# Kernel optimization log

Hardware: AMD Instinct MI355X
Metric: run time of the kernel (lower is better)

Reference implementation:

```python
import jax, jax.numpy as jnp
import numpy as np

EMBED_DIM = 1024
NUM_HEADS = 16
HEAD_DIM = EMBED_DIM // NUM_HEADS


def setup_inputs() -> dict:
    key = jax.random.key(0)
    ks = jax.random.split(key, 7)
    B, S, D = 2, 2048, EMBED_DIM
    s = 1.0 / np.sqrt(D)
    return {
        "x": jax.random.normal(ks[0], (B, S, D), dtype=jnp.float32),
        "Wq": jax.random.normal(ks[1], (D, D), dtype=jnp.float32) * s,
        "bq": jax.random.normal(ks[2], (D,), dtype=jnp.float32) * 0.01,
        "Wk": jax.random.normal(ks[3], (D, D), dtype=jnp.float32) * s,
        "bk": jax.random.normal(ks[4], (D,), dtype=jnp.float32) * 0.01,
        "Wv": jax.random.normal(ks[5], (D, D), dtype=jnp.float32) * s,
        "bv": jax.random.normal(ks[6], (D,), dtype=jnp.float32) * 0.01,
    }


def reference(x, Wq, bq, Wk, bk, Wv, bv):
    B, S, D = x.shape
    H, Hd = NUM_HEADS, HEAD_DIM
    # QKV projections, then split heads: [B, S, D] -> [B, H, S, Hd]
    q = (x @ Wq + bq).reshape(B, S, H, Hd).transpose(0, 2, 1, 3)
    k = (x @ Wk + bk).reshape(B, S, H, Hd).transpose(0, 2, 1, 3)
    v = (x @ Wv + bv).reshape(B, S, H, Hd).transpose(0, 2, 1, 3)
    # NOTE: the original module applies NO 1/sqrt(head_dim) scaling.
    energy = jnp.einsum("bhqd,bhkd->bhqk", q, k)  # [B, H, S, S]
    attn = jax.nn.softmax(energy, axis=-1)
    out = jnp.einsum("bhqk,bhkd->bhqd", attn, v)
    return out.transpose(0, 2, 1, 3).reshape(B, S, D)
```

## Files before the change

kernel.cpp:

```cpp
#include <hip/hip_runtime.h>
#include <stdint.h>
#include <stddef.h>

typedef _Float16 half_t;
typedef __attribute__((ext_vector_type(8))) _Float16 h16x8;
typedef __attribute__((ext_vector_type(4))) _Float16 h16x4;
typedef __attribute__((ext_vector_type(4))) float f32x4;

#define MFMA16(a, b, c) __builtin_amdgcn_mfma_f32_16x16x32_f16(a, b, c, 0, 0, 0)
#define EXP2(x) __builtin_amdgcn_exp2f(x)

#define SW(row, slot) ((((slot) ^ ((row) & 7))) * 8)

__device__ __forceinline__ void gload_lds16(const half_t* g, half_t* l) {
    __builtin_amdgcn_global_load_lds(
        (const __attribute__((address_space(1))) void*)g,
        (__attribute__((address_space(3))) void*)l, 16, 0, 0);
}

__global__ __launch_bounds__(256) void cvt_x_kernel(const float* __restrict__ x,
                                                    half_t* __restrict__ xh, int n8) {
    int i = blockIdx.x * blockDim.x + threadIdx.x;
    if (i >= n8) return;
    const float4* xv = (const float4*)x;
    float4 a = xv[i * 2 + 0];
    float4 b = xv[i * 2 + 1];
    h16x8 o;
    o[0] = (half_t)a.x; o[1] = (half_t)a.y; o[2] = (half_t)a.z; o[3] = (half_t)a.w;
    o[4] = (half_t)b.x; o[5] = (half_t)b.y; o[6] = (half_t)b.z; o[7] = (half_t)b.w;
    ((h16x8*)xh)[i] = o;
}

__global__ __launch_bounds__(256) void cvt_w_kernel(const float* __restrict__ Wq,
                                                    const float* __restrict__ Wk,
                                                    const float* __restrict__ Wv,
                                                    half_t* __restrict__ Wt) {
    __shared__ float t[32][33];
    const float* W = (blockIdx.z == 0) ? Wq : ((blockIdx.z == 1) ? Wk : Wv);
    int k0 = blockIdx.y * 32, n0 = blockIdx.x * 32;
    int tid = threadIdx.x;
    int r = tid >> 3;
    int c4 = (tid & 7) * 4;
    float4 v = *(const float4*)&W[(size_t)(k0 + r) * 1024 + n0 + c4];
    t[r][c4 + 0] = v.x; t[r][c4 + 1] = v.y; t[r][c4 + 2] = v.z; t[r][c4 + 3] = v.w;
    __syncthreads();
    half_t* o = Wt + (size_t)blockIdx.z * 1024 * 1024 + (size_t)(n0 + r) * 1024 + k0 + c4;
    h16x4 h;
    h[0] = (half_t)t[c4 + 0][r];
    h[1] = (half_t)t[c4 + 1][r];
    h[2] = (half_t)t[c4 + 2][r];
    h[3] = (half_t)t[c4 + 3][r];
    *(h16x4*)o = h;
}

__global__ __launch_bounds__(256, 3) void gemm_qkv_kernel(
    const half_t* __restrict__ xh,
    const half_t* __restrict__ Wt,
    const float* __restrict__ bq, const float* __restrict__ bk,
    const float* __restrict__ bv,
    half_t* __restrict__ qkv)
{
    const int p = blockIdx.z;
    const float* bias = (p == 0) ? bq : ((p == 1) ? bk : bv);
    const half_t* Wp = Wt + (size_t)p * 1024 * 1024;
    const int n0 = blockIdx.x * 128, m0 = blockIdx.y * 128;

    __shared__ half_t Al[128][64];
    __shared__ half_t Bl[128][64];

    const int tid = threadIdx.x;
    const int lane = tid & 63, wid = tid >> 6;
    const int wm = wid >> 1, wn = wid & 1;
    const int g = lane >> 4, r = lane & 15;

    const int lrow = lane >> 3;
    const int swzc = ((lane & 7) ^ lrow) * 8;

    f32x4 acc[4][4];
#pragma unroll
    for (int a = 0; a < 4; a++)
#pragma unroll
        for (int c = 0; c < 4; c++) acc[a][c] = (f32x4){0.f, 0.f, 0.f, 0.f};

    for (int k0 = 0; k0 < 1024; k0 += 64) {
        __syncthreads();
#pragma unroll
        for (int j = 0; j < 4; j++) {
            int issue = wid * 4 + j;
            int row = issue * 8 + lrow;
            gload_lds16(&xh[(size_t)(m0 + row) * 1024 + k0 + swzc], &Al[0][0] + issue * 512);
            gload_lds16(&Wp[(size_t)(n0 + row) * 1024 + k0 + swzc], &Bl[0][0] + issue * 512);
        }
        __syncthreads();

#pragma unroll
        for (int t = 0; t < 2; t++) {
            h16x8 af[4], bf[4];
#pragma unroll
            for (int mi = 0; mi < 4; mi++)
                af[mi] = *(const h16x8*)&Al[wm * 64 + mi * 16 + r][SW(r, t * 4 + g)];
#pragma unroll
            for (int ni = 0; ni < 4; ni++)
                bf[ni] = *(const h16x8*)&Bl[wn * 64 + ni * 16 + r][SW(r, t * 4 + g)];
#pragma unroll
            for (int mi = 0; mi < 4; mi++)
#pragma unroll
                for (int ni = 0; ni < 4; ni++)
                    acc[mi][ni] = MFMA16(af[mi], bf[ni], acc[mi][ni]);
        }
    }

    float bn[4];
#pragma unroll
    for (int ni = 0; ni < 4; ni++) bn[ni] = bias[n0 + wn * 64 + ni * 16 + r];

    if (p == 0) {
        half_t* outp = qkv;
#pragma unroll
        for (int mi = 0; mi < 4; mi++) {
#pragma unroll
            for (int ni = 0; ni < 4; ni++) {
                int n = n0 + wn * 64 + ni * 16 + r;
                int hq = n >> 6, hd = n & 63;
#pragma unroll
                for (int i = 0; i < 4; i++) {
                    int m = m0 + wm * 64 + mi * 16 + g * 4 + i;
                    int b = m >> 11, s = m & 2047;
                    outp[(((size_t)(b * 16 + hq) * 2048 + s) << 6) + hd] =
                        (half_t)(acc[mi][ni][i] + bn[ni]);
                }
            }
        }
    } else if (p == 1) {
        half_t* outp = qkv + (size_t)4194304;
        const int kt = ((m0 & 2047) + wm * 64) >> 6;
        const int bK = (m0 + wm * 64) >> 11;
#pragma unroll
        for (int ni = 0; ni < 4; ni++) {
            int n = n0 + wn * 64 + ni * 16 + r;
            int hK = n >> 6, hd = n & 63;
            int tt = hd >> 5, ggk = (hd >> 3) & 3, jK = hd & 7;
            size_t base = (size_t)(bK * 16 + hK) * 131072 + kt * 4096 + tt * 512 + ggk * 128 + jK;
#pragma unroll
            for (int mi = 0; mi < 4; mi++)
#pragma unroll
                for (int i = 0; i < 4; i++)
                    outp[base + mi * 1024 + (g * 4 + i) * 8] =
                        (half_t)(acc[mi][ni][i] + bn[ni]);
        }
    } else {
        half_t* outp = qkv + (size_t)2 * 4194304;
        const int kt = ((m0 & 2047) + wm * 64) >> 6;
        const int bV = (m0 + wm * 64) >> 11;
        const int jv = (g & 1) * 4, gv_hi = g >> 1;
#pragma unroll
        for (int ni = 0; ni < 4; ni++) {
            int n = n0 + wn * 64 + ni * 16 + r;
            int hV = n >> 6;
            size_t hb = (size_t)(bV * 16 + hV) * 131072 + kt * 4096 + ni * 1024;
#pragma unroll
            for (int mi = 0; mi < 4; mi++) {
                int ks = mi >> 1, ggv = (mi & 1) * 2 + gv_hi;
                h16x4 pk;
#pragma unroll
                for (int i = 0; i < 4; i++) pk[i] = (half_t)(acc[mi][ni][i] + bn[ni]);
                *(h16x4*)&outp[hb + ks * 512 + ggv * 128 + r * 8 + jv] = pk;
            }
        }
    }
}

__global__ __launch_bounds__(256, 2) void attn_kernel(
    const half_t* __restrict__ Qg,
    const half_t* __restrict__ Kswz,
    const half_t* __restrict__ Vswz,
    float* __restrict__ out)
{
    __shared__ half_t Pl[4][32][64];

    const int tid = threadIdx.x;
    const int lane = tid & 63, wid = tid >> 6;
    const int g = lane >> 4, r = lane & 15;

    const int bid = blockIdx.x;
    const int xcd = bid & 7;
    const int t_  = bid >> 3;
    const int qblk = t_ & 15;
    const int bh = xcd + 8 * (t_ >> 4);

    const int b = bh >> 4, h = bh & 15;
    const half_t* Qb = Qg + (size_t)bh * 131072;
    const half_t* Kp = Kswz + (size_t)bh * 131072;
    const half_t* Vp = Vswz + (size_t)bh * 131072;
    const int q0 = qblk * 128 + wid * 32;
    const int lofs = g * 128 + r * 8;

    h16x8 qf[2][2];
#pragma unroll
    for (int qg = 0; qg < 2; qg++)
#pragma unroll
        for (int t = 0; t < 2; t++) {
            qf[qg][t] = *(const h16x8*)&Qb[(size_t)(q0 + qg * 16 + r) * 64 + t * 32 + g * 8];
            qf[qg][t] *= (half_t)1.44269504f;
        }

    const h16x8 ones = {(half_t)1.f, (half_t)1.f, (half_t)1.f, (half_t)1.f,
                        (half_t)1.f, (half_t)1.f, (half_t)1.f, (half_t)1.f};

    f32x4 o[2][4], lsum[2];
#pragma unroll
    for (int qg = 0; qg < 2; qg++) {
#pragma unroll
        for (int d = 0; d < 4; d++) o[qg][d] = (f32x4){0.f, 0.f, 0.f, 0.f};
        lsum[qg] = (f32x4){0.f, 0.f, 0.f, 0.f};
    }
    float m_run[2] = {0.f, 0.f};

    h16x8 kf[8], vf[8];

    auto loadK = [&](int kt) {
#pragma unroll
        for (int kc = 0; kc < 4; kc++)
#pragma unroll
            for (int t = 0; t < 2; t++)
                kf[kc * 2 + t] = *(const h16x8*)&Kp[kt * 4096 + kc * 1024 + t * 512 + lofs];
    };
    auto loadV = [&](int kt) {
#pragma unroll
        for (int d = 0; d < 4; d++)
#pragma unroll
            for (int ks = 0; ks < 2; ks++)
                vf[d * 2 + ks] = *(const h16x8*)&Vp[kt * 4096 + d * 1024 + ks * 512 + lofs];
    };

    auto QKT = [&](f32x4 (&e)[2][4]) {
        __builtin_amdgcn_s_setprio(1);
#pragma unroll
        for (int kc = 0; kc < 4; kc++) {
            e[0][kc] = (f32x4){0.f, 0.f, 0.f, 0.f};
            e[1][kc] = (f32x4){0.f, 0.f, 0.f, 0.f};
#pragma unroll
            for (int t = 0; t < 2; t++) {
                e[0][kc] = MFMA16(kf[kc * 2 + t], qf[0][t], e[0][kc]);
                e[1][kc] = MFMA16(kf[kc * 2 + t], qf[1][t], e[1][kc]);
            }
        }
        __builtin_amdgcn_s_setprio(0);
    };

    auto SOFTMAX_P = [&](f32x4 (&e)[2][4]) {
#pragma unroll
        for (int qg = 0; qg < 2; qg++) {
            float t0 = fmaxf(fmaxf(e[qg][0][0], e[qg][0][1]), e[qg][0][2]);
            float t1 = fmaxf(fmaxf(e[qg][0][3], e[qg][1][0]), e[qg][1][1]);
            float t2 = fmaxf(fmaxf(e[qg][1][2], e[qg][1][3]), e[qg][2][0]);
            float t3 = fmaxf(fmaxf(e[qg][2][1], e[qg][2][2]), e[qg][2][3]);
            float t4 = fmaxf(fmaxf(e[qg][3][0], e[qg][3][1]), e[qg][3][2]);
            float tm = fmaxf(fmaxf(t0, t1), fmaxf(fmaxf(t2, t3), fmaxf(t4, e[qg][3][3])));
            tm = fmaxf(tm, __shfl_xor(tm, 16));
            tm = fmaxf(tm, __shfl_xor(tm, 32));

#pragma unroll
            for (int kc = 0; kc < 4; kc++)
#pragma unroll
                for (int i = 0; i < 4; i++) e[qg][kc][i] = EXP2(e[qg][kc][i] - m_run[qg]);

            if (!__all(tm <= m_run[qg] + 8.f)) {
                float nm = fmaxf(m_run[qg], tm);
                float sc = EXP2(m_run[qg] - nm);
                m_run[qg] = nm;
#pragma unroll
                for (int kc = 0; kc < 4; kc++)
#pragma unroll
                    for (int i = 0; i < 4; i++) e[qg][kc][i] *= sc;
#pragma unroll
                for (int i = 0; i < 4; i++) {
                    float sci = __shfl(sc, (lane & 48) | (g * 4 + i));
                    lsum[qg][i] *= sci;
#pragma unroll
                    for (int d = 0; d < 4; d++) o[qg][d][i] *= sci;
                }
            }

#pragma unroll
            for (int kc = 0; kc < 4; kc++) {
                h16x4 pk;
#pragma unroll
                for (int i = 0; i < 4; i++) pk[i] = (half_t)e[qg][kc][i];
                *(h16x4*)&Pl[wid][qg * 16 + r][SW(r, 2 * kc + (g >> 1)) + (g & 1) * 4] = pk;
            }
        }
    };

    auto PV = [&]() {
        asm volatile("s_waitcnt lgkmcnt(0)" ::: "memory");
        __builtin_amdgcn_sched_barrier(0);
        __builtin_amdgcn_s_setprio(1);
#pragma unroll
        for (int ks = 0; ks < 2; ks++) {
            h16x8 pf0 = *(const h16x8*)&Pl[wid][r][SW(r, ks * 4 + g)];
            h16x8 pf1 = *(const h16x8*)&Pl[wid][16 + r][SW(r, ks * 4 + g)];
#pragma unroll
            for (int d = 0; d < 4; d++) {
                o[0][d] = MFMA16(pf0, vf[d * 2 + ks], o[0][d]);
                o[1][d] = MFMA16(pf1, vf[d * 2 + ks], o[1][d]);
            }
            lsum[0] = MFMA16(pf0, ones, lsum[0]);
            lsum[1] = MFMA16(pf1, ones, lsum[1]);
        }
        __builtin_amdgcn_s_setprio(0);
    };

    f32x4 eA[2][4], eB[2][4];
    loadK(0);
    QKT(eA);
    loadK(1);

    for (int kt = 0; kt < 32; kt += 2) {
        loadV(kt);
        SOFTMAX_P(eA);
        QKT(eB);
        loadK((kt + 2) & 31);
        PV();
        loadV(kt + 1);
        SOFTMAX_P(eB);
        QKT(eA);
        loadK((kt + 3) & 31);
        PV();
    }

#pragma unroll
    for (int qg = 0; qg < 2; qg++)
#pragma unroll
        for (int i = 0; i < 4; i++) {
            float inv = 1.0f / lsum[qg][i];
            int s = q0 + qg * 16 + g * 4 + i;
            float* op = out + (size_t)(b * 2048 + s) * 1024 + h * 64 + r;
#pragma unroll
            for (int d = 0; d < 4; d++) op[d * 16] = o[qg][d][i] * inv;
        }
}

extern "C" void kernel_launch(void* const* d_in, const int* in_sizes, int n_in,
                              void* d_out, int out_size, void* d_ws, size_t ws_size,
                              hipStream_t stream) {
    const float* x  = (const float*)d_in[0];
    const float* Wq = (const float*)d_in[1];
    const float* bq = (const float*)d_in[2];
    const float* Wk = (const float*)d_in[3];
    const float* bk = (const float*)d_in[4];
    const float* Wv = (const float*)d_in[5];
    const float* bv = (const float*)d_in[6];
    float* out = (float*)d_out;

    half_t* xh  = (half_t*)d_ws;
    half_t* Wt  = (half_t*)((char*)d_ws + (size_t)8 * 1024 * 1024);
    half_t* qkv = (half_t*)((char*)d_ws + (size_t)14 * 1024 * 1024);
    half_t* Qh  = qkv;
    half_t* Kh  = qkv + (size_t)4194304;
    half_t* Vth = qkv + (size_t)8388608;

    cvt_x_kernel<<<2048, 256, 0, stream>>>(x, xh, 524288);
    cvt_w_kernel<<<dim3(32, 32, 3), 256, 0, stream>>>(Wq, Wk, Wv, Wt);
    gemm_qkv_kernel<<<dim3(8, 32, 3), 256, 0, stream>>>(xh, Wt, bq, bk, bv, qkv);
    attn_kernel<<<512, 256, 0, stream>>>(Qh, Kh, Vth, out);
}
```

Baseline: 98.65 us.

## Feed P to PV MFMA directly from registers, dropping LDS round-trip

Softmax probabilities are now kept in registers and fed straight to 16x16x16 MFMAs for the PV product, so the per-wave LDS staging buffer, its writes, waitcnt and reads are gone. The V output layout in the projection kernel is rearranged so the accumulator layout of QK^T matches the B operand of the K=16 MFMA. In exchange it doubles the number of PV MFMA instructions at half the K depth, and it reorders the pipeline so softmax runs after the next QK^T is issued.

```diff
diff --git a/kernel.cpp b/kernel.cpp
--- a/kernel.cpp
+++ b/kernel.cpp
@@ -7,7 +7,8 @@
 typedef __attribute__((ext_vector_type(4))) _Float16 h16x4;
 typedef __attribute__((ext_vector_type(4))) float f32x4;
 
-#define MFMA16(a, b, c) __builtin_amdgcn_mfma_f32_16x16x32_f16(a, b, c, 0, 0, 0)
+#define MFMA16(a, b, c)   __builtin_amdgcn_mfma_f32_16x16x32_f16(a, b, c, 0, 0, 0)
+#define MFMA16K16(a, b, c) __builtin_amdgcn_mfma_f32_16x16x16f16(a, b, c, 0, 0, 0)
 #define EXP2(x) __builtin_amdgcn_exp2f(x)
 
 #define SW(row, slot) ((((slot) ^ ((row) & 7))) * 8)
@@ -152,19 +153,16 @@
         half_t* outp = qkv + (size_t)2 * 4194304;
         const int kt = ((m0 & 2047) + wm * 64) >> 6;
         const int bV = (m0 + wm * 64) >> 11;
-        const int jv = (g & 1) * 4, gv_hi = g >> 1;
+        const int hV = (n0 + wn * 64) >> 6;
+        size_t base = (size_t)(bV * 16 + hV) * 131072 + kt * 4096 + (g * 16 + r) * 8;
 #pragma unroll
         for (int ni = 0; ni < 4; ni++) {
-            int n = n0 + wn * 64 + ni * 16 + r;
-            int hV = n >> 6;
-            size_t hb = (size_t)(bV * 16 + hV) * 131072 + kt * 4096 + ni * 1024;
 #pragma unroll
             for (int mi = 0; mi < 4; mi++) {
-                int ks = mi >> 1, ggv = (mi & 1) * 2 + gv_hi;
                 h16x4 pk;
 #pragma unroll
                 for (int i = 0; i < 4; i++) pk[i] = (half_t)(acc[mi][ni][i] + bn[ni]);
-                *(h16x4*)&outp[hb + ks * 512 + ggv * 128 + r * 8 + jv] = pk;
+                *(h16x4*)&outp[base + (ni * 2 + (mi >> 1)) * 512 + (mi & 1) * 4] = pk;
             }
         }
     }
@@ -176,10 +174,8 @@
     const half_t* __restrict__ Vswz,
     float* __restrict__ out)
 {
-    __shared__ half_t Pl[4][32][64];
-
     const int tid = threadIdx.x;
-    const int lane = tid & 63, wid = tid >> 6;
+    const int lane = tid & 63;
     const int g = lane >> 4, r = lane & 15;
 
     const int bid = blockIdx.x;
@@ -192,7 +188,7 @@
     const half_t* Qb = Qg + (size_t)bh * 131072;
     const half_t* Kp = Kswz + (size_t)bh * 131072;
     const half_t* Vp = Vswz + (size_t)bh * 131072;
-    const int q0 = qblk * 128 + wid * 32;
+    const int q0 = qblk * 128 + (tid >> 6) * 32;
     const int lofs = g * 128 + r * 8;
 
     h16x8 qf[2][2];
@@ -204,8 +200,7 @@
             qf[qg][t] *= (half_t)1.44269504f;
         }
 
-    const h16x8 ones = {(half_t)1.f, (half_t)1.f, (half_t)1.f, (half_t)1.f,
-                        (half_t)1.f, (half_t)1.f, (half_t)1.f, (half_t)1.f};
+    const h16x4 ones4 = {(half_t)1.f, (half_t)1.f, (half_t)1.f, (half_t)1.f};
 
     f32x4 o[2][4], lsum[2];
 #pragma unroll
@@ -227,10 +222,8 @@
     };
     auto loadV = [&](int kt) {
 #pragma unroll
-        for (int d = 0; d < 4; d++)
-#pragma unroll
-            for (int ks = 0; ks < 2; ks++)
-                vf[d * 2 + ks] = *(const h16x8*)&Vp[kt * 4096 + d * 1024 + ks * 512 + lofs];
+        for (int dh = 0; dh < 8; dh++)
+            vf[dh] = *(const h16x8*)&Vp[kt * 4096 + dh * 512 + lofs];
     };
 
     auto QKT = [&](f32x4 (&e)[2][4]) {
@@ -248,7 +241,8 @@
         __builtin_amdgcn_s_setprio(0);
     };
 
-    auto SOFTMAX_P = [&](f32x4 (&e)[2][4]) {
+    auto SOFTMAX_PV = [&](f32x4 (&e)[2][4]) {
+        h16x4 pk[2][4];
 #pragma unroll
         for (int qg = 0; qg < 2; qg++) {
             float t0 = fmaxf(fmaxf(e[qg][0][0], e[qg][0][1]), e[qg][0][2]);
@@ -283,30 +277,25 @@
             }
 
 #pragma unroll
-            for (int kc = 0; kc < 4; kc++) {
-                h16x4 pk;
-#pragma unroll
-                for (int i = 0; i < 4; i++) pk[i] = (half_t)e[qg][kc][i];
-                *(h16x4*)&Pl[wid][qg * 16 + r][SW(r, 2 * kc + (g >> 1)) + (g & 1) * 4] = pk;
-            }
-        }
-    };
-
-    auto PV = [&]() {
-        asm volatile("s_waitcnt lgkmcnt(0)" ::: "memory");
-        __builtin_amdgcn_sched_barrier(0);
+            for (int kc = 0; kc < 4; kc++)
+#pragma unroll
+                for (int i = 0; i < 4; i++) pk[qg][kc][i] = (half_t)e[qg][kc][i];
+        }
+
         __builtin_amdgcn_s_setprio(1);
 #pragma unroll
-        for (int ks = 0; ks < 2; ks++) {
-            h16x8 pf0 = *(const h16x8*)&Pl[wid][r][SW(r, ks * 4 + g)];
-            h16x8 pf1 = *(const h16x8*)&Pl[wid][16 + r][SW(r, ks * 4 + g)];
+        for (int kc = 0; kc < 4; kc++) {
 #pragma unroll
             for (int d = 0; d < 4; d++) {
-                o[0][d] = MFMA16(pf0, vf[d * 2 + ks], o[0][d]);
-                o[1][d] = MFMA16(pf1, vf[d * 2 + ks], o[1][d]);
-            }
-            lsum[0] = MFMA16(pf0, ones, lsum[0]);
-            lsum[1] = MFMA16(pf1, ones, lsum[1]);
+                const h16x8 vreg = vf[d * 2 + (kc >> 1)];
+                const h16x4 vv = (kc & 1)
+                    ? __builtin_shufflevector(vreg, vreg, 4, 5, 6, 7)
+                    : __builtin_shufflevector(vreg, vreg, 0, 1, 2, 3);
+                o[0][d] = MFMA16K16(pk[0][kc], vv, o[0][d]);
+                o[1][d] = MFMA16K16(pk[1][kc], vv, o[1][d]);
+            }
+            lsum[0] = MFMA16K16(pk[0][kc], ones4, lsum[0]);
+            lsum[1] = MFMA16K16(pk[1][kc], ones4, lsum[1]);
         }
         __builtin_amdgcn_s_setprio(0);
     };
@@ -318,15 +307,13 @@
 
     for (int kt = 0; kt < 32; kt += 2) {
         loadV(kt);
-        SOFTMAX_P(eA);
         QKT(eB);
         loadK((kt + 2) & 31);
-        PV();
+        SOFTMAX_PV(eA);
         loadV(kt + 1);
-        SOFTMAX_P(eB);
         QKT(eA);
         loadK((kt + 3) & 31);
-        PV();
+        SOFTMAX_PV(eB);
     }
 
 #pragma unroll
```

New measurement: 104.4 us. +5.8%, slower.
